# Optimization experiments

Measured on AMD Instinct MI355X. Metric: run time of the kernel, lower is better.

## Reference

```python
import jax, jax.numpy as jnp
import numpy as np

RADIUS = 4          # config.corr_radius
LEVELS = 4          # config.corr_levels
EPS = 1e-12         # torch F.normalize eps


def _avg_pool(x, s):
    # exact equivalent of F.avg_pool2d(x, s, stride=s) when H,W divisible by s
    if s == 1:
        return x
    B, C, H, W = x.shape
    return x.reshape(B, C, H // s, s, W // s, s).mean(axis=(3, 5))


def _l2_normalize_c(x):
    # F.normalize(x, dim=1): x / max(||x||_2, eps)
    n = jnp.sqrt(jnp.sum(x * x, axis=1, keepdims=True))
    return x / jnp.maximum(n, EPS)


def _corr_volume(f1, f2, r):
    # windowed correlation: corr[:, idx, y, x] = sum_c f1[:,c,y,x] * f2[:,c,y-dy,x-dx]
    # (zero padding outside), idx iterates dy outer, dx inner, each in [-r, r]
    B, C, H, W = f1.shape
    f1n = _l2_normalize_c(f1)
    f2n = _l2_normalize_c(f2)
    f2p = jnp.pad(f2n, ((0, 0), (0, 0), (r, r), (r, r)))
    corrs = []
    for dy in range(-r, r + 1):
        for dx in range(-r, r + 1):
            sl = f2p[:, :, r - dy:r - dy + H, r - dx:r - dx + W]  # shifted fmap2
            corrs.append(jnp.einsum('bchw,bchw->bhw', f1n, sl))
    return jnp.stack(corrs, axis=1)  # [B, (2r+1)^2, H, W]


def setup_inputs() -> dict:
    key = jax.random.key(0)
    k1, k2, k3, k4 = jax.random.split(key, 4)
    B, C, H, W = 4, 256, 160, 160
    return {
        'fmap1': jax.random.normal(k1, (B, C, H, W), dtype=jnp.float32),
        'fmap2': jax.random.normal(k2, (B, C, H, W), dtype=jnp.float32),
        'depth1': jax.random.uniform(k3, (B, 1, H, W), dtype=jnp.float32),
        'depth2': jax.random.uniform(k4, (B, 1, H, W), dtype=jnp.float32),
        'depth_w': jnp.float32(0.1),  # learned depth_correlation_weight param
    }


def reference(fmap1, fmap2, depth1, depth2, depth_w):
    pyramid = []
    for i in range(LEVELS):
        s = 2 ** i
        f1 = _avg_pool(fmap1, s)
        f2 = _avg_pool(fmap2, s)
        corr = _corr_volume(f1, f2, RADIUS)  # [B, 81, h, w]
        d1 = _avg_pool(depth1, s)
        d2 = _avg_pool(depth2, s)
        depth_corr = jnp.exp(-jnp.abs(d1 - d2))  # [B, 1, h, w], broadcasts over 81 channels
        pyramid.append(corr + depth_w * depth_corr)
    return tuple(pyramid)
```

## Files before the change

kernel.cpp:

```cpp
#include <hip/hip_runtime.h>
#include <hip/hip_bf16.h>


#define B_ 4
#define C_ 256
#define ND_ 81

typedef float  f32x4 __attribute__((ext_vector_type(4)));
typedef float  f32x2 __attribute__((ext_vector_type(2)));
typedef unsigned int u32x4 __attribute__((ext_vector_type(4)));
typedef __bf16 bf16x8 __attribute__((ext_vector_type(8)));
typedef unsigned short u16x4 __attribute__((ext_vector_type(4)));

__device__ __forceinline__ unsigned short f2bf(float f) {
  unsigned int u = __builtin_bit_cast(unsigned int, f);
  u += 0x7FFFu + ((u >> 16) & 1u);
  return (unsigned short)(u >> 16);
}

__device__ __forceinline__ void gload16(const void* g, void* l) {
  __builtin_amdgcn_global_load_lds(
      (const __attribute__((address_space(1))) unsigned int*)g,
      (__attribute__((address_space(3))) unsigned int*)l, 16, 0, 0);
}

template<int Ho, int Wo>
__global__ __launch_bounds__(256) void pool16(
    const float* __restrict__ f1i, const float* __restrict__ f2i,
    const float* __restrict__ d1i, const float* __restrict__ d2i,
    float* __restrict__ f1o, float* __restrict__ f2o,
    float* __restrict__ d1o, float* __restrict__ d2o) {
  constexpr long HWo = (long)Ho * Wo;
  constexpr long G4F = (long)B_ * C_ * HWo / 4;
  constexpr long G4D = (long)B_ * HWo / 4;
  constexpr long N   = 2 * G4F + 2 * G4D;
  constexpr long TT  = N / 4;
  long t = (long)blockIdx.x * blockDim.x + threadIdx.x;
  if (t >= TT) return;

  f32x4 va[4][4];
  float* dsts[4];
  long   gs[4];

#pragma unroll
  for (int j = 0; j < 4; ++j) {
    long g = t + (long)j * TT;
    const float* src; float* dst;
    if      (g < G4F)           { src = f1i; dst = f1o; }
    else if (g < 2*G4F)         { src = f2i; dst = f2o; g -= G4F; }
    else if (g < 2*G4F + G4D)   { src = d1i; dst = d1o; g -= 2*G4F; }
    else                        { src = d2i; dst = d2o; g -= 2*G4F + G4D; }
    constexpr long GP = HWo / 4;
    long plane = g / GP;
    long gp    = g - plane * GP;
    int  yo    = (int)(gp / (Wo / 4));
    int  xg    = (int)(gp - (long)yo * (Wo / 4));
    constexpr int Wi = 2 * Wo;
    const float* p0 = src + (plane * (2 * Ho) + 2 * yo) * (long)Wi + 8 * xg;
    va[j][0] = *(const f32x4*)p0;
    va[j][1] = *(const f32x4*)(p0 + 4);
    va[j][2] = *(const f32x4*)(p0 + Wi);
    va[j][3] = *(const f32x4*)(p0 + Wi + 4);
    dsts[j] = dst;
    gs[j]   = g;
  }

#pragma unroll
  for (int j = 0; j < 4; ++j) {
    f32x4 o;
    o.x = 0.25f * (va[j][0].x + va[j][0].y + va[j][2].x + va[j][2].y);
    o.y = 0.25f * (va[j][0].z + va[j][0].w + va[j][2].z + va[j][2].w);
    o.z = 0.25f * (va[j][1].x + va[j][1].y + va[j][3].x + va[j][3].y);
    o.w = 0.25f * (va[j][1].z + va[j][1].w + va[j][3].z + va[j][3].w);
    *(f32x4*)(dsts[j] + 4 * gs[j]) = o;
  }
}

template<int W>
__global__ __launch_bounds__(256) void norm_tp2(
    const float* __restrict__ src1, const float* __restrict__ src2,
    unsigned short* __restrict__ dst1, unsigned short* __restrict__ dst2) {
  constexpr int HW = W * W, Wp = W + 8;
  __shared__ unsigned short raw[64 * 260];
  __shared__ float ssp[4][64];
  __shared__ float inv[64];
  int tid = threadIdx.x;
  int lane = tid & 63, w = tid >> 6;
  long pix0 = (long)blockIdx.x * 64;
  int z = blockIdx.z, b = z >> 1;
  bool pad = (z & 1) != 0;
  const float* src = pad ? src2 : src1;
  unsigned short* dst = pad ? dst2 : dst1;
  bool ok = (pix0 + lane) < HW;
  const float* base = src + (long)b * C_ * HW + pix0 + lane;

  float ss = 0.f;
  float vv[16];
  for (int cb = 0; cb < 64; cb += 16) {
    int c0 = w * 64 + cb;
#pragma unroll
    for (int j = 0; j < 16; ++j)
      vv[j] = ok ? base[(long)(c0 + j) * HW] : 0.f;
#pragma unroll
    for (int g = 0; g < 4; ++g) {
      u16x4 pk;
#pragma unroll
      for (int j = 0; j < 4; ++j) {
        float v = vv[g * 4 + j];
        ss += v * v;
        pk[j] = f2bf(v);
      }
      *(u16x4*)&raw[lane * 260 + c0 + g * 4] = pk;
    }
  }
  ssp[w][lane] = ss;
  __syncthreads();
  if (tid < 64) {
    float s = ssp[0][tid] + ssp[1][tid] + ssp[2][tid] + ssp[3][tid];
    inv[tid] = 1.f / fmaxf(sqrtf(s), 1e-12f);
  }
  __syncthreads();

  int c4 = lane * 4;
  for (int p = w; p < 64; p += 4) {
    long pix = pix0 + p;
    if (pix < HW) {
      long off;
      if (pad) {
        int y = (int)(pix / W);
        int x = (int)(pix - (long)y * W);
        off = (((long)b * Wp + (y + 4)) * Wp + (x + 4)) * C_ + c4;
      } else {
        off = ((long)b * HW + pix) * C_ + c4;
      }
      u16x4 r = *(const u16x4*)&raw[p * 260 + c4];
      float sc = inv[p];
      u16x4 o;
#pragma unroll
      for (int j = 0; j < 4; ++j) {
        float v = __builtin_bit_cast(float, ((unsigned int)r[j]) << 16) * sc;
        o[j] = f2bf(v);
      }
      *(u16x4*)&dst[off] = o;
    }
  }
}

__global__ __launch_bounds__(256) void norm_tp_c(
    const float* __restrict__ src1, const float* __restrict__ src2,
    unsigned short* __restrict__ dst1, unsigned short* __restrict__ dst2, int HW_) {
  __shared__ unsigned short raw[64 * 260];
  __shared__ float ssp[4][64];
  __shared__ float inv[64];
  int tid = threadIdx.x;
  int lane = tid & 63, w = tid >> 6;
  long HW = HW_;
  long pix0 = (long)blockIdx.x * 64;
  int z = blockIdx.z, b = z >> 1;
  const float* src = (z & 1) ? src2 : src1;
  unsigned short* dst = (z & 1) ? dst2 : dst1;
  bool ok = (pix0 + lane) < HW;
  const float* base = src + (long)b * C_ * HW + pix0 + lane;

  float ss = 0.f;
  float vv[16];
  for (int cb = 0; cb < 64; cb += 16) {
    int c0 = w * 64 + cb;
#pragma unroll
    for (int j = 0; j < 16; ++j)
      vv[j] = ok ? base[(long)(c0 + j) * HW] : 0.f;
#pragma unroll
    for (int g = 0; g < 4; ++g) {
      u16x4 pk;
#pragma unroll
      for (int j = 0; j < 4; ++j) {
        float v = vv[g * 4 + j];
        ss += v * v;
        pk[j] = f2bf(v);
      }
      *(u16x4*)&raw[lane * 260 + c0 + g * 4] = pk;
    }
  }
  ssp[w][lane] = ss;
  __syncthreads();
  if (tid < 64) {
    float s = ssp[0][tid] + ssp[1][tid] + ssp[2][tid] + ssp[3][tid];
    inv[tid] = 1.f / fmaxf(sqrtf(s), 1e-12f);
  }
  __syncthreads();
  int c4 = lane * 4;
  unsigned short* dbase = dst + ((long)b * HW + pix0) * C_;
  for (int p = w; p < 64; p += 4) {
    if (pix0 + p < HW) {
      u16x4 r = *(const u16x4*)&raw[p * 260 + c4];
      float sc = inv[p];
      u16x4 o;
#pragma unroll
      for (int j = 0; j < 4; ++j) {
        float v = __builtin_bit_cast(float, ((unsigned int)r[j]) << 16) * sc;
        o[j] = f2bf(v);
      }
      *(u16x4*)&dbase[(long)p * C_ + c4] = o;
    }
  }
}

template<int W>
__global__ void zero_halo(unsigned short* __restrict__ fp) {
  constexpr int Wp = W + 8;
  constexpr long UN = (long)B_ * Wp * Wp * 32;
  long u = (long)blockIdx.x * 256 + threadIdx.x;
  if (u >= UN) return;
  long px = u >> 5;
  long pp = px % ((long)Wp * Wp);
  int y = (int)(pp / Wp), x = (int)(pp - (long)(pp / Wp) * Wp);
  if (y < 4 || y >= Wp - 4 || x < 4 || x >= Wp - 4) {
    u16x4 z4 = {0, 0, 0, 0};
    *(u16x4*)&fp[u * 8] = z4;
  }
}

template<int W>
__global__ __launch_bounds__(256, 3) void corr2(
    const unsigned short* __restrict__ f1n, const unsigned short* __restrict__ f2pd,
    const float* __restrict__ d1, const float* __restrict__ d2,
    const float* __restrict__ dwp, float* __restrict__ out) {
  constexpr int H = W, Wp = W + 8, Hp = H + 8;
  constexpr int GX = (W + 15) / 16, GY = H / 4;
  constexpr int NB = GX * GY * B_;
  constexpr int CPX = NB / 8;
  constexpr int BUFB = 18944;
  __shared__ char smem[2 * BUFB];
  unsigned short* sb = (unsigned short*)smem;

  int tid = threadIdx.x;
  int lane = tid & 63, wv = tid >> 6;
  int n16 = lane & 15, hi = lane >> 4;

  int f = blockIdx.x;
  int nf = (f & 7) * CPX + (f >> 3);
  int j = nf % GY;
  int rest = nf / GY;
  int i = rest % GX;
  int b = rest / GX;
  int x0 = i * 16, y0 = j * 4, y = y0 + wv;
  long HW = (long)W * H;

  int xm = x0 + n16;
  bool aok = xm < W;
  const unsigned short* abase = f1n + ((long)b * HW + (long)y * W + xm) * C_ + hi * 8;
  bf16x8 afr[8];
#pragma unroll
  for (int kc = 0; kc < 8; ++kc) {
    u32x4 rr = {0u, 0u, 0u, 0u};
    if (aok) rr = *(const u32x4*)(abase + kc * 32);
    afr[kc] = __builtin_bit_cast(bf16x8, rr);
  }

  const char* gbase = (const char*)f2pd;
  long gb[5];
#pragma unroll
  for (int it = 0; it < 5; ++it) {
    int u = tid + it * 256;
    int u2 = (u < 1152) ? u : 0;
    int sl = (u2 & ~7) | ((u2 & 7) ^ ((u2 >> 3) & 7));
    int px = sl >> 2, s = sl & 3;
    int row = px / 24, col = px - row * 24;
    int gx = x0 + col; if (gx > Wp - 1) gx = Wp - 1;
    int gy = y0 + row;
    gb[it] = (((long)b * Hp + gy) * Wp + gx) * 512 + s * 16;
  }

  f32x4 acc[9][2];
#pragma unroll
  for (int dy = 0; dy < 9; ++dy)
#pragma unroll
    for (int nt = 0; nt < 2; ++nt)
      acc[dy][nt] = f32x4{0.f, 0.f, 0.f, 0.f};

#pragma unroll
  for (int it = 0; it < 5; ++it)
    if (tid + it * 256 < 1152)
      gload16(gbase + gb[it], smem + (tid + it * 256) * 16);
  __syncthreads();

#pragma unroll
  for (int kc = 0; kc < 8; ++kc) {
    int cur = kc & 1;
    if (kc < 7) {
      char* dstb = smem + (cur ^ 1) * BUFB;
#pragma unroll
      for (int it = 0; it < 5; ++it)
        if (tid + it * 256 < 1152)
          gload16(gbase + gb[it] + (long)(kc + 1) * 64, dstb + (tid + it * 256) * 16);
    }
    const unsigned short* bufc = sb + cur * (BUFB / 2);
#pragma unroll
    for (int dy = 0; dy < 9; ++dy) {
      int rbase = (wv + dy) * 96;
#pragma unroll
      for (int nt = 0; nt < 2; ++nt) {
        int sl = rbase + (nt * 16 + n16) * 4 + hi;
        int ph = (sl & ~7) | ((sl & 7) ^ ((sl >> 3) & 7));
        bf16x8 bfr = *(const bf16x8*)(bufc + ph * 8);
        acc[dy][nt] = __builtin_amdgcn_mfma_f32_16x16x32_bf16(afr[kc], bfr, acc[dy][nt], 0, 0, 0);
      }
    }
    __syncthreads();
  }

  float* lds_o = (float*)smem;
  float* dt = (float*)(smem + 64 * ND_ * 4);
#pragma unroll
  for (int dy = 0; dy < 9; ++dy)
#pragma unroll
    for (int nt = 0; nt < 2; ++nt)
#pragma unroll
      for (int r = 0; r < 4; ++r) {
        int m = hi * 4 + r;
        int dx = nt * 16 + n16 - m - 4;
        if (dx >= -4 && dx <= 4) {
          int d = (8 - dy) * 9 + (4 - dx);
          lds_o[(wv * 16 + m) * ND_ + d] = acc[dy][nt][r];
        }
      }
  if (tid < 64) {
    int ty = tid >> 4, tx = tid & 15;
    int xq = x0 + tx, yq = y0 + ty;
    float v = 0.f;
    if (xq < W) {
      long pidx = (long)b * HW + (long)yq * W + xq;
      v = dwp[0] * expf(-fabsf(d1[pidx] - d2[pidx]));
    }
    dt[tid] = v;
  }
  __syncthreads();
  long obase = (long)b * ND_ * HW;
  for (int it = 0; it < 21; ++it) {
    int flat = it * 256 + tid;
    if (flat < 64 * ND_) {
      int d = flat >> 6;
      int p = flat & 63;
      int xq = x0 + (p & 15);
      if (xq < W)
        out[obase + (long)d * HW + (long)(y0 + (p >> 4)) * W + xq] = lds_o[p * ND_ + d] + dt[p];
    }
  }
}

__global__ __launch_bounds__(256, 2) void corr_g(
    const unsigned short* __restrict__ f1n, const unsigned short* __restrict__ f2n,
    const float* __restrict__ d1, const float* __restrict__ d2,
    const float* __restrict__ dwp, float* __restrict__ out, int H, int W) {
  __shared__ float lds_o[64 * ND_];
  __shared__ float dt[64];
  int tid = threadIdx.x;
  int lane = tid & 63, wv = tid >> 6;
  int x0 = blockIdx.x * 16, y0 = blockIdx.y * 4, b = blockIdx.z;
  int y = y0 + wv;
  int n16 = lane & 15, hi = lane >> 4;
  long HW = (long)H * W;

  int xm = x0 + n16;
  bool aok = xm < W;
  const unsigned short* abase = f1n + ((long)b * HW + (long)y * W + xm) * C_ + hi * 8;
  bf16x8 afr[8];
#pragma unroll
  for (int ch = 0; ch < 8; ++ch) {
    u32x4 rr = {0u, 0u, 0u, 0u};
    if (aok) rr = *(const u32x4*)(abase + ch * 32);
    afr[ch] = __builtin_bit_cast(bf16x8, rr);
  }

  f32x4 acc[9][2];
#pragma unroll
  for (int dy = 0; dy < 9; ++dy)
#pragma unroll
    for (int nt = 0; nt < 2; ++nt)
      acc[dy][nt] = f32x4{0.f, 0.f, 0.f, 0.f};

#pragma unroll
  for (int dy = 0; dy < 9; ++dy) {
    int yy = y + dy - 4;
    if (yy >= 0 && yy < H) {
      const unsigned short* brow = f2n + ((long)b * HW + (long)yy * W) * C_;
#pragma unroll
      for (int nt = 0; nt < 2; ++nt) {
        int wx = x0 - 4 + nt * 16 + n16;
        bool bok = (wx >= 0) && (wx < W);
        const unsigned short* bbase = brow + (long)wx * C_ + hi * 8;
        bf16x8 bfr[8];
#pragma unroll
        for (int ch = 0; ch < 8; ++ch) {
          u32x4 rr = {0u, 0u, 0u, 0u};
          if (bok) rr = *(const u32x4*)(bbase + ch * 32);
          bfr[ch] = __builtin_bit_cast(bf16x8, rr);
        }
#pragma unroll
        for (int ch = 0; ch < 8; ++ch)
          acc[dy][nt] = __builtin_amdgcn_mfma_f32_16x16x32_bf16(afr[ch], bfr[ch], acc[dy][nt], 0, 0, 0);
      }
    }
  }

#pragma unroll
  for (int dy = 0; dy < 9; ++dy)
#pragma unroll
    for (int nt = 0; nt < 2; ++nt)
#pragma unroll
      for (int r = 0; r < 4; ++r) {
        int m = hi * 4 + r;
        int dx = nt * 16 + n16 - m - 4;
        if (dx >= -4 && dx <= 4) {
          int d = (8 - dy) * 9 + (4 - dx);
          lds_o[(wv * 16 + m) * ND_ + d] = acc[dy][nt][r];
        }
      }
  if (tid < 64) {
    int ty = tid >> 4, tx = tid & 15;
    int xq = x0 + tx, yq = y0 + ty;
    float v = 0.f;
    if (xq < W) {
      long pidx = (long)b * HW + (long)yq * W + xq;
      v = dwp[0] * expf(-fabsf(d1[pidx] - d2[pidx]));
    }
    dt[tid] = v;
  }
  __syncthreads();
  long obase = (long)b * ND_ * HW;
  for (int it = 0; it < 21; ++it) {
    int flat = it * 256 + tid;
    if (flat < 64 * ND_) {
      int d = flat >> 6;
      int p = flat & 63;
      int xq = x0 + (p & 15);
      if (xq < W)
        out[obase + (long)d * HW + (long)(y0 + (p >> 4)) * W + xq] = lds_o[p * ND_ + d] + dt[p];
    }
  }
}

extern "C" void kernel_launch(void* const* d_in, const int* in_sizes, int n_in,
                              void* d_out, int out_size, void* d_ws, size_t ws_size,
                              hipStream_t stream) {
  const float* f1  = (const float*)d_in[0];
  const float* f2  = (const float*)d_in[1];
  const float* dp1 = (const float*)d_in[2];
  const float* dp2 = (const float*)d_in[3];
  const float* dw  = (const float*)d_in[4];
  float* out = (float*)d_out;

  char* ws = (char*)d_ws;
  size_t off = 0;
  auto alloc = [&](size_t bytes) -> void* {
    void* p = ws + off;
    off = (off + bytes + 255) & ~(size_t)255;
    return p;
  };
  static const long HWs[4] = {25600, 6400, 1600, 400};
  float* f1p[4]; float* f2p[4]; float* d1p[4]; float* d2p[4];
  for (int l = 1; l <= 3; ++l) f1p[l] = (float*)alloc((size_t)B_ * C_ * HWs[l] * 4);
  for (int l = 1; l <= 3; ++l) f2p[l] = (float*)alloc((size_t)B_ * C_ * HWs[l] * 4);
  for (int l = 1; l <= 3; ++l) d1p[l] = (float*)alloc((size_t)B_ * HWs[l] * 4);
  for (int l = 1; l <= 3; ++l) d2p[l] = (float*)alloc((size_t)B_ * HWs[l] * 4);
  unsigned short* f1n0 = (unsigned short*)alloc((size_t)B_ * 25600 * C_ * 2);
  unsigned short* f1n1 = (unsigned short*)alloc((size_t)B_ * 6400 * C_ * 2);
  unsigned short* f2n0 = (unsigned short*)alloc((size_t)B_ * 168 * 168 * C_ * 2);
  unsigned short* f2n1 = (unsigned short*)alloc((size_t)B_ * 88 * 88 * C_ * 2);
  unsigned short* f1n2 = (unsigned short*)alloc((size_t)B_ * 1600 * C_ * 2);
  unsigned short* f2n2 = (unsigned short*)alloc((size_t)B_ * 1600 * C_ * 2);
  unsigned short* f1n3 = (unsigned short*)alloc((size_t)B_ * 400 * C_ * 2);
  unsigned short* f2n3 = (unsigned short*)alloc((size_t)B_ * 400 * C_ * 2);
  if (off > ws_size) return;

  pool16<80, 80><<<dim3(3213), 256, 0, stream>>>(
      f1, f2, dp1, dp2, f1p[1], f2p[1], d1p[1], d2p[1]);
  pool16<40, 40><<<dim3(804), 256, 0, stream>>>(
      f1p[1], f2p[1], d1p[1], d2p[1], f1p[2], f2p[2], d1p[2], d2p[2]);
  pool16<20, 20><<<dim3(201), 256, 0, stream>>>(
      f1p[2], f2p[2], d1p[2], d2p[2], f1p[3], f2p[3], d1p[3], d2p[3]);

  norm_tp2<160><<<dim3(400, 1, 8), 256, 0, stream>>>(f1, f2, f1n0, f2n0);
  norm_tp2< 80><<<dim3(100, 1, 8), 256, 0, stream>>>(f1p[1], f2p[1], f1n1, f2n1);
  zero_halo<160><<<dim3(14112), 256, 0, stream>>>(f2n0);
  zero_halo< 80><<<dim3( 3872), 256, 0, stream>>>(f2n1);
  corr2<160><<<dim3(1600), 256, 0, stream>>>(f1n0, f2n0, dp1,    dp2,    dw, out);
  corr2< 80><<<dim3( 400), 256, 0, stream>>>(f1n1, f2n1, d1p[1], d2p[1], dw, out + 8294400);

  norm_tp_c<<<dim3(25, 1, 8), 256, 0, stream>>>(f1p[2], f2p[2], f1n2, f2n2, 1600);
  norm_tp_c<<<dim3( 7, 1, 8), 256, 0, stream>>>(f1p[3], f2p[3], f1n3, f2n3, 400);
  corr_g<<<dim3(3, 10, 4), 256, 0, stream>>>(f1n2, f2n2, d1p[2], d2p[2], dw, out + 10368000, 40, 40);
  corr_g<<<dim3(2,  5, 4), 256, 0, stream>>>(f1n3, f2n3, d1p[3], d2p[3], dw, out + 10886400, 20, 20);
}
```

Baseline: 282.0 us.

## Fuse level-0 normalization/transpose with 2x2 average pooling of feature maps

Replaces the separate level-1 pooling pass and the level-0 normalize-transpose kernel with one kernel that reads each full-resolution fp32 feature tile once. It packs the tile to bf16 in shared memory for the normalized transpose and computes the 2x2 pooled outputs with lane shuffles. Depth pooling for level 1 moves to a small separate kernel. This removes a second full read of the largest input tensors. The cost is a different block shape (2 rows by 32 columns) and scattered strided pooled stores from only half the lanes.

```diff
diff --git a/kernel.cpp b/kernel.cpp
--- a/kernel.cpp
+++ b/kernel.cpp
@@ -22,6 +22,95 @@
   __builtin_amdgcn_global_load_lds(
       (const __attribute__((address_space(1))) unsigned int*)g,
       (__attribute__((address_space(3))) unsigned int*)l, 16, 0, 0);
+}
+
+__global__ __launch_bounds__(256) void norm_pool160(
+    const float* __restrict__ src1, const float* __restrict__ src2,
+    unsigned short* __restrict__ dst1, unsigned short* __restrict__ dst2,
+    float* __restrict__ pool1, float* __restrict__ pool2) {
+  constexpr int W = 160, HW = W * W, Wp = W + 8, W1 = 80, HW1 = W1 * W1;
+  __shared__ unsigned short raw[64 * 260];
+  __shared__ float ssp[4][64];
+  __shared__ float inv[64];
+  int tid = threadIdx.x;
+  int lane = tid & 63, w = tid >> 6;
+  int x0 = blockIdx.x * 32, y0 = blockIdx.y * 2;
+  int z = blockIdx.z, b = z >> 1;
+  bool pad = (z & 1) != 0;
+  const float* src = pad ? src2 : src1;
+  unsigned short* dst = pad ? dst2 : dst1;
+  float* pooled = pad ? pool2 : pool1;
+  int lr = lane >> 5, lc = lane & 31;
+  const float* base = src + (long)b * C_ * HW + (long)(y0 + lr) * W + x0 + lc;
+  long pbase = (long)b * C_ * HW1 + (long)(y0 >> 1) * W1 + (x0 >> 1);
+  bool pw = (lane < 32) && !(lane & 1);
+  int k = lane >> 1;
+
+  float ss = 0.f;
+  float vv[16];
+  for (int cb = 0; cb < 64; cb += 16) {
+    int c0 = w * 64 + cb;
+#pragma unroll
+    for (int j = 0; j < 16; ++j)
+      vv[j] = base[(long)(c0 + j) * HW];
+#pragma unroll
+    for (int g = 0; g < 4; ++g) {
+      u16x4 pk;
+#pragma unroll
+      for (int j = 0; j < 4; ++j) {
+        float v = vv[g * 4 + j];
+        ss += v * v;
+        pk[j] = f2bf(v);
+      }
+      *(u16x4*)&raw[lane * 260 + c0 + g * 4] = pk;
+    }
+#pragma unroll
+    for (int j = 0; j < 16; ++j) {
+      float t = vv[j] + __shfl_xor(vv[j], 1);
+      float q = t + __shfl_xor(t, 32);
+      if (pw) pooled[pbase + (long)(c0 + j) * HW1 + k] = 0.25f * q;
+    }
+  }
+  ssp[w][lane] = ss;
+  __syncthreads();
+  if (tid < 64) {
+    float s = ssp[0][tid] + ssp[1][tid] + ssp[2][tid] + ssp[3][tid];
+    inv[tid] = 1.f / fmaxf(sqrtf(s), 1e-12f);
+  }
+  __syncthreads();
+
+  int c4 = lane * 4;
+  for (int p = w; p < 64; p += 4) {
+    int y = y0 + (p >> 5), x = x0 + (p & 31);
+    long off;
+    if (pad) off = (((long)b * Wp + (y + 4)) * Wp + (x + 4)) * C_ + c4;
+    else     off = ((long)b * HW + (long)y * W + x) * C_ + c4;
+    u16x4 r = *(const u16x4*)&raw[p * 260 + c4];
+    float sc = inv[p];
+    u16x4 o;
+#pragma unroll
+    for (int j = 0; j < 4; ++j) {
+      float v = __builtin_bit_cast(float, ((unsigned int)r[j]) << 16) * sc;
+      o[j] = f2bf(v);
+    }
+    *(u16x4*)&dst[off] = o;
+  }
+}
+
+__global__ void pool_d1(const float* __restrict__ d1i, const float* __restrict__ d2i,
+                        float* __restrict__ d1o, float* __restrict__ d2o) {
+  constexpr int HWo = 6400, N = 2 * B_ * HWo;
+  int i = blockIdx.x * 256 + threadIdx.x;
+  if (i >= N) return;
+  const float* src = (i < B_ * HWo) ? d1i : d2i;
+  float* dst = (i < B_ * HWo) ? d1o : d2o;
+  int r = (i < B_ * HWo) ? i : i - B_ * HWo;
+  int pl = r / HWo, pix = r - pl * HWo;
+  int yo = pix / 80, xo = pix - yo * 80;
+  const float* p0 = src + ((long)pl * 160 + 2 * yo) * 160 + 2 * xo;
+  f32x2 a = *(const f32x2*)p0;
+  f32x2 c = *(const f32x2*)(p0 + 160);
+  dst[r] = 0.25f * (a.x + a.y + c.x + c.y);
 }
 
 template<int Ho, int Wo>
@@ -37,11 +126,9 @@
   constexpr long TT  = N / 4;
   long t = (long)blockIdx.x * blockDim.x + threadIdx.x;
   if (t >= TT) return;
-
   f32x4 va[4][4];
   float* dsts[4];
   long   gs[4];
-
 #pragma unroll
   for (int j = 0; j < 4; ++j) {
     long g = t + (long)j * TT;
@@ -64,7 +151,6 @@
     dsts[j] = dst;
     gs[j]   = g;
   }
-
 #pragma unroll
   for (int j = 0; j < 4; ++j) {
     f32x4 o;
@@ -473,14 +559,14 @@
   unsigned short* f2n3 = (unsigned short*)alloc((size_t)B_ * 400 * C_ * 2);
   if (off > ws_size) return;
 
-  pool16<80, 80><<<dim3(3213), 256, 0, stream>>>(
-      f1, f2, dp1, dp2, f1p[1], f2p[1], d1p[1], d2p[1]);
+  norm_pool160<<<dim3(5, 80, 8), 256, 0, stream>>>(f1, f2, f1n0, f2n0, f1p[1], f2p[1]);
+  pool_d1<<<dim3(200), 256, 0, stream>>>(dp1, dp2, d1p[1], d2p[1]);
+
   pool16<40, 40><<<dim3(804), 256, 0, stream>>>(
       f1p[1], f2p[1], d1p[1], d2p[1], f1p[2], f2p[2], d1p[2], d2p[2]);
   pool16<20, 20><<<dim3(201), 256, 0, stream>>>(
       f1p[2], f2p[2], d1p[2], d2p[2], f1p[3], f2p[3], d1p[3], d2p[3]);
 
-  norm_tp2<160><<<dim3(400, 1, 8), 256, 0, stream>>>(f1, f2, f1n0, f2n0);
   norm_tp2< 80><<<dim3(100, 1, 8), 256, 0, stream>>>(f1p[1], f2p[1], f1n1, f2n1);
   zero_halo<160><<<dim3(14112), 256, 0, stream>>>(f2n0);
   zero_halo< 80><<<dim3( 3872), 256, 0, stream>>>(f2n1);
```

After: 250.1 us. 11.3% less time.
